# Kernel tuning notes

Hardware: AMD Instinct MI355X
Metric: run time of the kernel (lower is better)

Reference implementation:

```python
import jax, jax.numpy as jnp
import numpy as np

FEAT_STRIDE = 8
IM_DIMS = (4096.0, 4096.0)  # (height, width)
ANCHOR_SCALES = (8.0, 16.0, 32.0)
RATIOS = (0.5, 1.0, 2.0)
PRE_NMS_TOPN = 12000   # TRAIN cfg (eval_mode=False)
POST_NMS_TOPN = 2000
NMS_THRESH = 0.7
MIN_SIZE = 16.0


def _generate_anchors(base_size=16.0, ratios=RATIOS, scales=ANCHOR_SCALES):
    ratios = np.array(ratios, np.float32)
    scales = np.array(scales, np.float32)
    w = h = float(base_size)
    x_ctr = 0.5 * (w - 1.0)
    y_ctr = 0.5 * (h - 1.0)
    size = w * h
    ws = np.round(np.sqrt(size / ratios))
    hs = np.round(ws * ratios)
    out = []
    for wr, hr in zip(ws, hs):
        wss = wr * scales
        hss = hr * scales
        out.append(np.stack([x_ctr - 0.5 * (wss - 1.0), y_ctr - 0.5 * (hss - 1.0),
                             x_ctr + 0.5 * (wss - 1.0), y_ctr + 0.5 * (hss - 1.0)], axis=1))
    return np.concatenate(out, 0).astype(np.float32)  # [A=9, 4]


def _nms(boxes, scores, thresh, max_out):
    # greedy sequential NMS; indices are discrete -> stop gradients here
    boxes = jax.lax.stop_gradient(boxes)
    scores = jax.lax.stop_gradient(scores)
    areas = (boxes[:, 2] - boxes[:, 0] + 1.0) * (boxes[:, 3] - boxes[:, 1] + 1.0)

    def body(i, state):
        supp, keep = state
        idx = jnp.argmax(jnp.where(supp, -jnp.inf, scores))
        b = boxes[idx]
        xx1 = jnp.maximum(b[0], boxes[:, 0])
        yy1 = jnp.maximum(b[1], boxes[:, 1])
        xx2 = jnp.minimum(b[2], boxes[:, 2])
        yy2 = jnp.minimum(b[3], boxes[:, 3])
        inter = jnp.maximum(0.0, xx2 - xx1 + 1.0) * jnp.maximum(0.0, yy2 - yy1 + 1.0)
        iou = inter / (areas[idx] + areas - inter)
        supp = supp | (iou > thresh)  # also suppresses idx itself (iou==1)
        keep = keep.at[i].set(idx.astype(jnp.int32))
        return supp, keep

    supp0 = jnp.zeros(boxes.shape[0], dtype=bool)
    keep0 = jnp.zeros(max_out, dtype=jnp.int32)
    _, keep = jax.lax.fori_loop(0, max_out, body, (supp0, keep0))
    return keep


def reference(rpn_cls_score, rpn_bbox_pred):
    _, H, W, C2 = rpn_cls_score.shape
    A = C2 // 2
    # rpn_softmax: per-anchor 2-way (bg, fg) softmax; channels laid out [2, A]
    prob = jax.nn.softmax(rpn_cls_score.reshape(H, W, 2, A), axis=2)
    scores = prob[:, :, 1, :].reshape(-1)           # fg scores, [H*W*A]
    deltas = rpn_bbox_pred.reshape(-1, 4)           # [H*W*A, 4]

    # anchors shifted over the feature grid
    anchors = jnp.asarray(_generate_anchors())       # [A, 4]
    sx = jnp.arange(W, dtype=jnp.float32) * FEAT_STRIDE
    sy = jnp.arange(H, dtype=jnp.float32) * FEAT_STRIDE
    shift_x, shift_y = jnp.meshgrid(sx, sy)          # [H, W]
    shifts = jnp.stack([shift_x, shift_y, shift_x, shift_y], -1).reshape(-1, 1, 4)
    all_anchors = (anchors[None, :, :] + shifts).reshape(-1, 4)  # [H*W*A, 4]

    # bbox_transform_inv
    ws = all_anchors[:, 2] - all_anchors[:, 0] + 1.0
    hs = all_anchors[:, 3] - all_anchors[:, 1] + 1.0
    cx = all_anchors[:, 0] + 0.5 * ws
    cy = all_anchors[:, 1] + 0.5 * hs
    dx, dy, dw, dh = deltas[:, 0], deltas[:, 1], deltas[:, 2], deltas[:, 3]
    pcx = dx * ws + cx
    pcy = dy * hs + cy
    pw = jnp.exp(dw) * ws
    ph = jnp.exp(dh) * hs
    x1 = pcx - 0.5 * pw
    y1 = pcy - 0.5 * ph
    x2 = pcx + 0.5 * pw
    y2 = pcy + 0.5 * ph

    # clip to image boundaries
    x1 = jnp.clip(x1, 0.0, IM_DIMS[1] - 1.0)
    y1 = jnp.clip(y1, 0.0, IM_DIMS[0] - 1.0)
    x2 = jnp.clip(x2, 0.0, IM_DIMS[1] - 1.0)
    y2 = jnp.clip(y2, 0.0, IM_DIMS[0] - 1.0)
    proposals = jnp.stack([x1, y1, x2, y2], axis=1)

    # drop tiny boxes (jit-friendly: -inf score instead of physical removal)
    keep_min = ((x2 - x1 + 1.0) >= MIN_SIZE) & ((y2 - y1 + 1.0) >= MIN_SIZE)
    scores = jnp.where(keep_min, scores, -jnp.inf)

    top_scores, order = jax.lax.top_k(scores, PRE_NMS_TOPN)
    props = proposals[order]                         # [pre_nms_topN, 4]
    keep = _nms(props, top_scores, NMS_THRESH, POST_NMS_TOPN)
    rois = props[keep]                               # [post_nms_topN, 4]
    # blob: [batch_idx(=0), x1, y1, x2, y2]
    return jnp.concatenate([jnp.zeros((POST_NMS_TOPN, 1), rois.dtype), rois], axis=1)


def setup_inputs() -> dict:
    key = jax.random.key(0)
    k1, k2 = jax.random.split(key)
    rpn_cls_score = jax.random.normal(k1, (1, 512, 512, 18), dtype=jnp.float32)
    rpn_bbox_pred = jax.random.normal(k2, (1, 512, 512, 36), dtype=jnp.float32) * 0.2
    return {"rpn_cls_score": rpn_cls_score, "rpn_bbox_pred": rpn_bbox_pred}
```

## Files before the change

kernel.cpp:

```cpp
#include <hip/hip_runtime.h>
#include <cstdint>
#include <cstddef>

#pragma clang fp contract(off)

#define N_ANCH 2359296
#define K_PRE  12000
#define K_POST 2000
#define NWORD  188
#define TIE_CAP 65536

typedef unsigned int u32;
typedef unsigned long long u64;

__constant__ float c_anch[9][4] = {
  { -84.f,  -40.f,   99.f,   55.f },
  { -176.f, -88.f,  191.f,  103.f },
  { -360.f, -184.f, 375.f,  199.f },
  { -56.f,  -56.f,   71.f,   71.f },
  { -120.f, -120.f, 135.f,  135.f },
  { -248.f, -248.f, 263.f,  263.f },
  { -36.f,  -80.f,   51.f,   95.f },
  { -80.f,  -168.f,  95.f,  183.f },
  { -168.f, -344.f, 183.f,  359.f },
};

__device__ __forceinline__ float pexpf(float xin) {
#pragma clang fp contract(off)
  const float exp_hi = 88.3762626647950f;
  const float exp_lo = -88.3762626647949f;
  const float LOG2EF = 1.44269504088896341f;
  const float C1 = 0.693359375f;
  const float C2 = -2.12194440e-4f;
  const float p0 = 1.9875691500E-4f;
  const float p1 = 1.3981999507E-3f;
  const float p2 = 8.3334519073E-3f;
  const float p3 = 4.1665795894E-2f;
  const float p4 = 1.6666665459E-1f;
  const float p5 = 5.0000001201E-1f;
  float x = fminf(fmaxf(xin, exp_lo), exp_hi);
  float fx = floorf(x * LOG2EF + 0.5f);
  float tmp = C1 * fx;
  float z = C2 * fx;
  x = x - tmp;
  x = x - z;
  z = x * x;
  float y = x * p0 + p1;
  y = y * x + p2;
  y = y * x + p3;
  y = y * x + p4;
  y = y * x + p5;
  y = y * z + x;
  y = 1.0f + y;
  int n = (int)fx;
  u32 e = ((u32)(n + 127)) << 23;
  return y * __uint_as_float(e);
}

__device__ __forceinline__ void decode_box(const float* __restrict__ bbox, int aidx,
                                           float4* ob, float* oarea, bool* okeep) {
#pragma clang fp contract(off)
  int pos = aidx / 9;
  int a = aidx - pos * 9;
  int w = pos & 511;
  int h = pos >> 9;
  float shx = (float)(w * 8);
  float shy = (float)(h * 8);
  float ax1 = c_anch[a][0] + shx;
  float ay1 = c_anch[a][1] + shy;
  float ax2 = c_anch[a][2] + shx;
  float ay2 = c_anch[a][3] + shy;
  float aw = (ax2 - ax1) + 1.0f;
  float ah = (ay2 - ay1) + 1.0f;
  float acx = ax1 + 0.5f * aw;
  float acy = ay1 + 0.5f * ah;
  const float* d = bbox + (size_t)pos * 36 + (size_t)a * 4;
  float dx = d[0], dy = d[1], dw = d[2], dh = d[3];
  float pcx = dx * aw + acx;
  float pcy = dy * ah + acy;
  float pw = pexpf(dw) * aw;
  float ph = pexpf(dh) * ah;
  float x1 = pcx - 0.5f * pw;
  float y1 = pcy - 0.5f * ph;
  float x2 = pcx + 0.5f * pw;
  float y2 = pcy + 0.5f * ph;
  x1 = fminf(fmaxf(x1, 0.0f), 4095.0f);
  y1 = fminf(fmaxf(y1, 0.0f), 4095.0f);
  x2 = fminf(fmaxf(x2, 0.0f), 4095.0f);
  y2 = fminf(fmaxf(y2, 0.0f), 4095.0f);
  *ob = make_float4(x1, y1, x2, y2);
  float ww = (x2 - x1) + 1.0f;
  float hh = (y2 - y1) + 1.0f;
  *oarea = ww * hh;
  *okeep = (ww >= 16.0f) && (hh >= 16.0f);
}

__global__ void k_scores(const float* __restrict__ cls, const float* __restrict__ bbox,
                         u32* __restrict__ keys, u32* __restrict__ ctl,
                         u32* __restrict__ hist) {
#pragma clang fp contract(off)
  int t = blockIdx.x * blockDim.x + threadIdx.x;
  if (blockIdx.x == 0) {
    if (threadIdx.x < 16) ctl[threadIdx.x] = (threadIdx.x == 1) ? (u32)K_PRE : 0u;
    hist[threadIdx.x] = 0u;
  }
  if (t >= N_ANCH) return;
  int pos = t / 9;
  int a = t - pos * 9;
  float s0 = cls[(size_t)pos * 18 + a];
  float s1 = cls[(size_t)pos * 18 + 9 + a];
  float m = fmaxf(s0, s1);
  float e0 = pexpf(s0 - m);
  float e1 = pexpf(s1 - m);
  float p = e1 / (e0 + e1);
  float4 box; float area; bool km;
  decode_box(bbox, t, &box, &area, &km);
  keys[t] = km ? (__float_as_uint(p) | 0x80000000u) : 0u;
}

__global__ void k_histscan(const u32* __restrict__ keys, u32* __restrict__ ctl,
                           u32* __restrict__ hist, int shift, int pass) {
  __shared__ u32 lh[256];
  __shared__ u32 s_last;
  int t = threadIdx.x;
  lh[t] = 0u;
  __syncthreads();
  u32 prefix = ctl[0];
  u32 msk = (shift == 24) ? 0u : (0xFFFFFFFFu << (shift + 8));
  int stride = gridDim.x * blockDim.x;
  for (int i = blockIdx.x * blockDim.x + t; i < N_ANCH; i += stride) {
    u32 k = keys[i];
    if ((k & msk) == prefix) atomicAdd(&lh[(k >> shift) & 0xFFu], 1u);
  }
  __syncthreads();
  if (lh[t]) atomicAdd(&hist[t], lh[t]);
  __syncthreads();
  if (t == 0) {
    __threadfence();
    u32 old = atomicAdd(&ctl[8 + pass], 1u);
    s_last = (old == gridDim.x - 1) ? 1u : 0u;
  }
  __syncthreads();
  if (!s_last) return;
  __threadfence();
  __shared__ u32 sh[256];
  __shared__ u32 horig[256];
  __shared__ int s_d;
  u32 h = atomicAdd(&hist[t], 0u);
  sh[t] = h; horig[t] = h;
  if (t == 0) s_d = 0;
  u32 krem = ctl[1];
  __syncthreads();
  u32 v = h;
  for (int off = 1; off < 256; off <<= 1) {
    u32 add = (t + off < 256) ? sh[t + off] : 0u;
    __syncthreads();
    v += add;
    sh[t] = v;
    __syncthreads();
  }
  if (sh[t] >= krem) atomicMax(&s_d, t);
  __syncthreads();
  if (t == 0) {
    int d = s_d;
    u32 cum = sh[d] - horig[d];
    ctl[0] |= ((u32)d) << shift;
    ctl[1] = krem - cum;
    if (shift == 0) { ctl[2] = ctl[0]; ctl[3] = ctl[1]; }
  }
  hist[t] = 0u;
}

__global__ void k_collect(const u32* __restrict__ keys, u32* __restrict__ ctl,
                          int* __restrict__ sel, int* __restrict__ tie,
                          u64* __restrict__ comps) {
  __shared__ int stI[2048];
  __shared__ u64 stC[2048];
  __shared__ int stT[256];
  __shared__ u32 s_cnt, s_tcnt, s_base, s_tbase;
  int tid = threadIdx.x;
  if (tid == 0) { s_cnt = 0; s_tcnt = 0; }
  __syncthreads();
  u32 kstar = ctl[2];
  int stride = gridDim.x * blockDim.x;
  for (int i = blockIdx.x * blockDim.x + tid; i < N_ANCH; i += stride) {
    u32 k = keys[i];
    if (k > kstar) {
      u32 p = atomicAdd(&s_cnt, 1u);
      u64 cmp = ((u64)k << 32) | (u64)(0xFFFFFFFFu - (u32)i);
      if (p < 2048u) { stI[p] = i; stC[p] = cmp; }
      else { u32 g = atomicAdd(&ctl[4], 1u); sel[g] = i; comps[g] = cmp; }
    } else if (k == kstar) {
      u32 p = atomicAdd(&s_tcnt, 1u);
      if (p < 256u) stT[p] = i;
      else { u32 g = atomicAdd(&ctl[5], 1u); if (g < TIE_CAP) tie[g] = i; }
    }
  }
  __syncthreads();
  if (tid == 0) {
    u32 n = min(s_cnt, 2048u);
    s_base = atomicAdd(&ctl[4], n);
    u32 tn = min(s_tcnt, 256u);
    s_tbase = atomicAdd(&ctl[5], tn);
  }
  __syncthreads();
  u32 n = min(s_cnt, 2048u);
  for (u32 q = tid; q < n; q += blockDim.x) {
    sel[s_base + q] = stI[q];
    comps[s_base + q] = stC[q];
  }
  u32 tn = min(s_tcnt, 256u);
  for (u32 q = tid; q < tn; q += blockDim.x) {
    u32 g = s_tbase + q;
    if (g < TIE_CAP) tie[g] = stT[q];
  }
}

__global__ void k_tiepick(const u32* __restrict__ ctl, const int* __restrict__ tie,
                          int* __restrict__ sel, u64* __restrict__ comps) {
  u32 T = ctl[5]; if (T > TIE_CAP) T = TIE_CAP;
  if (T > 8192u) T = 8192u;
  u32 need = ctl[3];
  u32 base = ctl[4];
  u32 kstar = ctl[2];
  for (u32 t = threadIdx.x; t < T; t += blockDim.x) {
    int v = tie[t];
    u32 r = 0;
    for (u32 u = 0; u < T; ++u) r += (tie[u] < v) ? 1u : 0u;
    if (r < need) {
      sel[base + r] = v;
      comps[base + r] = ((u64)kstar << 32) | (u64)(0xFFFFFFFFu - (u32)v);
    }
  }
}

__global__ void k_rankdec(const u64* __restrict__ comps, const int* __restrict__ sel,
                          const float* __restrict__ bbox,
                          float4* __restrict__ props, float* __restrict__ areas) {
  int lane = threadIdx.x & 63;
  int wave = threadIdx.x >> 6;
  int base = (blockIdx.x * 4 + wave) * 8;
  u64 c0 = comps[base + 0], c1 = comps[base + 1], c2 = comps[base + 2], c3 = comps[base + 3];
  u64 c4 = comps[base + 4], c5 = comps[base + 5], c6 = comps[base + 6], c7 = comps[base + 7];
  int n0 = 0, n1 = 0, n2 = 0, n3 = 0, n4 = 0, n5 = 0, n6 = 0, n7 = 0;
#pragma unroll 4
  for (int j = lane; j < K_PRE; j += 64) {
    u64 v = comps[j];
    n0 += (v > c0); n1 += (v > c1); n2 += (v > c2); n3 += (v > c3);
    n4 += (v > c4); n5 += (v > c5); n6 += (v > c6); n7 += (v > c7);
  }
  for (int off = 32; off; off >>= 1) {
    n0 += __shfl_xor(n0, off); n1 += __shfl_xor(n1, off);
    n2 += __shfl_xor(n2, off); n3 += __shfl_xor(n3, off);
    n4 += __shfl_xor(n4, off); n5 += __shfl_xor(n5, off);
    n6 += __shfl_xor(n6, off); n7 += __shfl_xor(n7, off);
  }
  int rk = n0;
  rk = (lane == 1) ? n1 : rk; rk = (lane == 2) ? n2 : rk;
  rk = (lane == 3) ? n3 : rk; rk = (lane == 4) ? n4 : rk;
  rk = (lane == 5) ? n5 : rk; rk = (lane == 6) ? n6 : rk;
  rk = (lane == 7) ? n7 : rk;
  if (lane < 8) {
    float4 box; float area; bool km;
    decode_box(bbox, sel[base + lane], &box, &area, &km);
    props[rk] = box;
    areas[rk] = area;
  }
}

__global__ void k_mask(const float4* __restrict__ props, const float* __restrict__ areas,
                       u64* __restrict__ mask, u64* __restrict__ diagbuf,
                       u64* __restrict__ subbuf) {
#pragma clang fp contract(off)
  int x = blockIdx.x, y = blockIdx.y;
  if (y + 1 < x || y == x + 1) return;
  __shared__ float4 bj[64];
  __shared__ float aj[64];
  int j0 = y * 64;
  bj[threadIdx.x] = props[j0 + threadIdx.x];
  aj[threadIdx.x] = areas[j0 + threadIdx.x];
  __syncthreads();
  int i = x * 64 + threadIdx.x;
  float4 bi = props[i];
  float ai = areas[i];
  u64 bits = 0;
  for (int jj = 0; jj < 64; ++jj) {
    int j = j0 + jj;
    float4 bb = bj[jj];
    float xx1 = fmaxf(bi.x, bb.x);
    float yy1 = fmaxf(bi.y, bb.y);
    float xx2 = fminf(bi.z, bb.z);
    float yy2 = fminf(bi.w, bb.w);
    float w = fmaxf(0.0f, (xx2 - xx1) + 1.0f);
    float h = fmaxf(0.0f, (yy2 - yy1) + 1.0f);
    float inter = w * h;
    float iou = inter / ((ai + aj[jj]) - inter);
    if ((iou > 0.7f) && (j < K_PRE)) bits |= (1ull << jj);
  }
  if (y == x)          diagbuf[x * 64 + threadIdx.x] = bits;
  else if (y == x - 1) subbuf[x * 64 + threadIdx.x] = bits;
  else                 mask[(size_t)i * NWORD + y] = bits;
}

#define NMS_BAR() asm volatile("s_waitcnt lgkmcnt(0)\n\ts_barrier" ::: "memory")

__global__ void __launch_bounds__(1024) k_nms(const u64* __restrict__ mask,
                                              const u64* __restrict__ diagbuf,
                                              const u64* __restrict__ subbuf,
                                              const float4* __restrict__ props,
                                              float* __restrict__ out) {
  __shared__ u64 rem[NWORD];
  __shared__ int keepb[K_POST];
  __shared__ int kept[2][64];
  __shared__ int s_kk[2];
  __shared__ int s_nk;
  __shared__ int s_brk;
  int tid = threadIdx.x;
  int lane = tid & 63;
  int wave = tid >> 6;
  for (int w = tid; w < NWORD; w += 1024) {
    int base = w * 64;
    u64 v;
    if (base + 64 <= K_PRE) v = 0ull;
    else if (base >= K_PRE) v = ~0ull;
    else v = (~0ull) << (K_PRE - base);
    rem[w] = v;
  }
  if (tid == 0) { s_nk = 0; s_brk = 0; s_kk[0] = 0; s_kk[1] = 0; }
  __syncthreads();

  u64 diagA = 0, diagB = 0, subA = 0, subB = 0;
  if (wave == 0) {
    diagA = diagbuf[lane];
    subA  = subbuf[64 + lane];
  }
  int nk = 0;

  for (int c = 0; c < NWORD; ++c) {
    if (s_brk) break;
    if (wave == 0) {
      if (c + 1 < NWORD) diagB = diagbuf[(c + 1) * 64 + lane];
      subB = (c + 2 < NWORD) ? subbuf[(c + 2) * 64 + lane] : 0ull;
      u64 w = ~rem[c];
      u64 myrow = diagA;
      int kk = 0;
      u64 km = 0;
      while (w != 0ull && nk < K_POST) {
        int j = (int)__builtin_ctzll(w);
        if (lane == 0) { keepb[nk] = (c << 6) | j; kept[c & 1][kk] = (c << 6) | j; }
        km |= (1ull << j);
        nk++; kk++;
        u64 sup = __ballot((int)((myrow >> j) & 1ull));
        w &= ~sup;
        w &= ~(1ull << j);
      }
      if (c + 1 < NWORD) {
        u64 v = __ballot((int)((subA & km) != 0ull));
        if (lane == 0 && v) atomicOr((unsigned long long*)&rem[c + 1], (unsigned long long)v);
      }
      if (lane == 0) {
        s_kk[c & 1] = kk;
        s_nk = nk;
        if (nk >= K_POST) s_brk = 1;
      }
      diagA = diagB; subA = subB;
    } else if (c >= 1) {
      int kkp = s_kk[(c - 1) & 1];
      const int* kb = &kept[(c - 1) & 1][0];
      int wv = wave - 1;
      int nu = kkp * 3;
      for (int b = wv; b < nu; b += 60) {
        int u0 = b, u1 = b + 15, u2 = b + 30, u3 = b + 45;
        u64 p0 = 0, p1 = 0, p2 = 0, p3 = 0;
        int w0 = 0, w1 = 0, w2 = 0, w3 = 0;
        if (u0 < nu) {
          int q = u0 / 3, s = u0 - q * 3;
          int w = c + 1 + s * 64 + lane;
          if (w < NWORD) { w0 = w; p0 = mask[(size_t)kb[q] * NWORD + w]; }
        }
        if (u1 < nu) {
          int q = u1 / 3, s = u1 - q * 3;
          int w = c + 1 + s * 64 + lane;
          if (w < NWORD) { w1 = w; p1 = mask[(size_t)kb[q] * NWORD + w]; }
        }
        if (u2 < nu) {
          int q = u2 / 3, s = u2 - q * 3;
          int w = c + 1 + s * 64 + lane;
          if (w < NWORD) { w2 = w; p2 = mask[(size_t)kb[q] * NWORD + w]; }
        }
        if (u3 < nu) {
          int q = u3 / 3, s = u3 - q * 3;
          int w = c + 1 + s * 64 + lane;
          if (w < NWORD) { w3 = w; p3 = mask[(size_t)kb[q] * NWORD + w]; }
        }
        if (p0) atomicOr((unsigned long long*)&rem[w0], (unsigned long long)p0);
        if (p1) atomicOr((unsigned long long*)&rem[w1], (unsigned long long)p1);
        if (p2) atomicOr((unsigned long long*)&rem[w2], (unsigned long long)p2);
        if (p3) atomicOr((unsigned long long*)&rem[w3], (unsigned long long)p3);
      }
    }
    NMS_BAR();
  }
  __syncthreads();
  int fnk = s_nk;
  for (int t = tid; t < K_POST; t += 1024) {
    int kidx = (t < fnk) ? keepb[t] : 0;
    float4 b = props[kidx];
    out[t * 5 + 0] = 0.0f;
    out[t * 5 + 1] = b.x;
    out[t * 5 + 2] = b.y;
    out[t * 5 + 3] = b.z;
    out[t * 5 + 4] = b.w;
  }
}

extern "C" void kernel_launch(void* const* d_in, const int* in_sizes, int n_in,
                              void* d_out, int out_size, void* d_ws, size_t ws_size,
                              hipStream_t stream) {
  const float* cls  = (const float*)d_in[0];
  const float* bbox = (const float*)d_in[1];
  float* out = (float*)d_out;
  char* ws = (char*)d_ws;

  u64* mask    = (u64*)ws;
  u32* keys    = (u32*)ws;
  u32* ctl     = (u32*)(ws + 9437184);
  u32* hist    = (u32*)(ws + 9437248);
  int* sel     = (int*)(ws + 9438464);
  int* tie     = (int*)(ws + 9486592);
  u64* comps   = (u64*)(ws + 18096128);
  float4* props= (float4*)(ws + 18240512);
  float* areas = (float*)(ws + 18433024);
  u64* diagbuf = (u64*)(ws + 18481152);
  u64* subbuf  = (u64*)(ws + 18577408);

  k_scores<<<dim3((N_ANCH + 255) / 256), dim3(256), 0, stream>>>(cls, bbox, keys, ctl, hist);
  const int shifts[4] = {24, 16, 8, 0};
  for (int s = 0; s < 4; ++s)
    k_histscan<<<dim3(256), dim3(256), 0, stream>>>(keys, ctl, hist, shifts[s], s);
  k_collect<<<dim3(256), dim3(256), 0, stream>>>(keys, ctl, sel, tie, comps);
  k_tiepick<<<dim3(1), dim3(256), 0, stream>>>(ctl, tie, sel, comps);
  k_rankdec<<<dim3(375), dim3(256), 0, stream>>>(comps, sel, bbox, props, areas);
  k_mask<<<dim3(188, 188), dim3(64), 0, stream>>>(props, areas, mask, diagbuf, subbuf);
  k_nms<<<dim3(1), dim3(1024), 0, stream>>>(mask, diagbuf, subbuf, props, out);
}
```

Baseline: 365.3 us.

## Fuse top-byte histogram into scores kernel and process NMS in 128-box chunks

The first radix-select histogram pass (top byte) is folded into k_scores through per-block shared histograms and a last-block scan, which removes one full pass over the keys. Counter initialisation moves to a small k_init kernel. The sequential NMS wave now handles two 64-bit words (128 boxes) per iteration, using 2x2 diagonal and sub-diagonal blocks, which halves the number of barrier-synchronised iterations of the serial loop. In exchange the scores kernel gains atomics and a grid-wide last-block step, and the serial wave does more ballots per iteration.

```diff
diff --git a/kernel.cpp b/kernel.cpp
--- a/kernel.cpp
+++ b/kernel.cpp
@@ -8,6 +8,7 @@
 #define K_PRE  12000
 #define K_POST 2000
 #define NWORD  188
+#define NC     94
 #define TIE_CAP 65536
 
 typedef unsigned int u32;
@@ -95,16 +96,22 @@
   *okeep = (ww >= 16.0f) && (hh >= 16.0f);
 }
 
+__global__ void k_init(u32* __restrict__ ctl, u32* __restrict__ hist) {
+  int t = threadIdx.x;
+  if (t < 16) ctl[t] = (t == 1) ? (u32)K_PRE : 0u;
+  hist[t] = 0u;
+}
+
 __global__ void k_scores(const float* __restrict__ cls, const float* __restrict__ bbox,
                          u32* __restrict__ keys, u32* __restrict__ ctl,
                          u32* __restrict__ hist) {
 #pragma clang fp contract(off)
-  int t = blockIdx.x * blockDim.x + threadIdx.x;
-  if (blockIdx.x == 0) {
-    if (threadIdx.x < 16) ctl[threadIdx.x] = (threadIdx.x == 1) ? (u32)K_PRE : 0u;
-    hist[threadIdx.x] = 0u;
-  }
-  if (t >= N_ANCH) return;
+  __shared__ u32 lh[256];
+  __shared__ u32 s_last;
+  int tid = threadIdx.x;
+  int t = blockIdx.x * blockDim.x + tid;
+  lh[tid] = 0u;
+  __syncthreads();
   int pos = t / 9;
   int a = t - pos * 9;
   float s0 = cls[(size_t)pos * 18 + a];
@@ -115,7 +122,45 @@
   float p = e1 / (e0 + e1);
   float4 box; float area; bool km;
   decode_box(bbox, t, &box, &area, &km);
-  keys[t] = km ? (__float_as_uint(p) | 0x80000000u) : 0u;
+  u32 key = km ? (__float_as_uint(p) | 0x80000000u) : 0u;
+  keys[t] = key;
+  atomicAdd(&lh[key >> 24], 1u);
+  __syncthreads();
+  if (lh[tid]) atomicAdd(&hist[tid], lh[tid]);
+  __syncthreads();
+  if (tid == 0) {
+    __threadfence();
+    u32 old = atomicAdd(&ctl[15], 1u);
+    s_last = (old == gridDim.x - 1) ? 1u : 0u;
+  }
+  __syncthreads();
+  if (!s_last) return;
+  __threadfence();
+  __shared__ u32 sh[256];
+  __shared__ u32 horig[256];
+  __shared__ int s_d;
+  u32 h = atomicAdd(&hist[tid], 0u);
+  sh[tid] = h; horig[tid] = h;
+  if (tid == 0) s_d = 0;
+  u32 krem = ctl[1];
+  __syncthreads();
+  u32 v = h;
+  for (int off = 1; off < 256; off <<= 1) {
+    u32 add = (tid + off < 256) ? sh[tid + off] : 0u;
+    __syncthreads();
+    v += add;
+    sh[tid] = v;
+    __syncthreads();
+  }
+  if (sh[tid] >= krem) atomicMax(&s_d, tid);
+  __syncthreads();
+  if (tid == 0) {
+    int d = s_d;
+    u32 cum = sh[d] - horig[d];
+    ctl[0] |= ((u32)d) << 24;
+    ctl[1] = krem - cum;
+  }
+  hist[tid] = 0u;
 }
 
 __global__ void k_histscan(const u32* __restrict__ keys, u32* __restrict__ ctl,
@@ -126,7 +171,7 @@
   lh[t] = 0u;
   __syncthreads();
   u32 prefix = ctl[0];
-  u32 msk = (shift == 24) ? 0u : (0xFFFFFFFFu << (shift + 8));
+  u32 msk = 0xFFFFFFFFu << (shift + 8);
   int stride = gridDim.x * blockDim.x;
   for (int i = blockIdx.x * blockDim.x + t; i < N_ANCH; i += stride) {
     u32 k = keys[i];
@@ -268,12 +313,17 @@
   }
 }
 
+__device__ __forceinline__ int d2idx(int c, int h, int lane) {
+  return ((c * 2 + h) * 64 + lane) * 2;
+}
+
 __global__ void k_mask(const float4* __restrict__ props, const float* __restrict__ areas,
-                       u64* __restrict__ mask, u64* __restrict__ diagbuf,
-                       u64* __restrict__ subbuf) {
+                       u64* __restrict__ mask, u64* __restrict__ diag2,
+                       u64* __restrict__ sub2) {
 #pragma clang fp contract(off)
   int x = blockIdx.x, y = blockIdx.y;
-  if (y + 1 < x || y == x + 1) return;
+  int cx = x >> 1, cy = y >> 1;
+  if (cy + 1 < cx || cy == cx + 1) return;
   __shared__ float4 bj[64];
   __shared__ float aj[64];
   int j0 = y * 64;
@@ -297,21 +347,21 @@
     float iou = inter / ((ai + aj[jj]) - inter);
     if ((iou > 0.7f) && (j < K_PRE)) bits |= (1ull << jj);
   }
-  if (y == x)          diagbuf[x * 64 + threadIdx.x] = bits;
-  else if (y == x - 1) subbuf[x * 64 + threadIdx.x] = bits;
-  else                 mask[(size_t)i * NWORD + y] = bits;
+  if (cy == cx)          diag2[d2idx(cx, x & 1, threadIdx.x) + (y & 1)] = bits;
+  else if (cy == cx - 1) sub2[d2idx(cx, x & 1, threadIdx.x) + (y & 1)] = bits;
+  else                   mask[(size_t)i * NWORD + y] = bits;
 }
 
 #define NMS_BAR() asm volatile("s_waitcnt lgkmcnt(0)\n\ts_barrier" ::: "memory")
 
 __global__ void __launch_bounds__(1024) k_nms(const u64* __restrict__ mask,
-                                              const u64* __restrict__ diagbuf,
-                                              const u64* __restrict__ subbuf,
+                                              const u64* __restrict__ diag2,
+                                              const u64* __restrict__ sub2,
                                               const float4* __restrict__ props,
                                               float* __restrict__ out) {
   __shared__ u64 rem[NWORD];
   __shared__ int keepb[K_POST];
-  __shared__ int kept[2][64];
+  __shared__ int kept[2][128];
   __shared__ int s_kk[2];
   __shared__ int s_nk;
   __shared__ int s_brk;
@@ -329,45 +379,76 @@
   if (tid == 0) { s_nk = 0; s_brk = 0; s_kk[0] = 0; s_kk[1] = 0; }
   __syncthreads();
 
-  u64 diagA = 0, diagB = 0, subA = 0, subB = 0;
+  u64 dl0A = 0, dl1A = 0, dh0A = 0, dh1A = 0;
+  u64 sl0A = 0, sl1A = 0, sh0A = 0, sh1A = 0;
+  u64 dl0B = 0, dl1B = 0, dh0B = 0, dh1B = 0;
+  u64 sl0B = 0, sl1B = 0, sh0B = 0, sh1B = 0;
   if (wave == 0) {
-    diagA = diagbuf[lane];
-    subA  = subbuf[64 + lane];
+    const u64* p;
+    p = diag2 + d2idx(0, 0, lane); dl0A = p[0]; dl1A = p[1];
+    p = diag2 + d2idx(0, 1, lane); dh0A = p[0]; dh1A = p[1];
+    p = sub2 + d2idx(1, 0, lane);  sl0A = p[0]; sl1A = p[1];
+    p = sub2 + d2idx(1, 1, lane);  sh0A = p[0]; sh1A = p[1];
   }
   int nk = 0;
 
-  for (int c = 0; c < NWORD; ++c) {
+  for (int c = 0; c < NC; ++c) {
     if (s_brk) break;
+    int par = c & 1;
     if (wave == 0) {
-      if (c + 1 < NWORD) diagB = diagbuf[(c + 1) * 64 + lane];
-      subB = (c + 2 < NWORD) ? subbuf[(c + 2) * 64 + lane] : 0ull;
-      u64 w = ~rem[c];
-      u64 myrow = diagA;
+      if (c + 1 < NC) {
+        const u64* p = diag2 + d2idx(c + 1, 0, lane); dl0B = p[0]; dl1B = p[1];
+        p = diag2 + d2idx(c + 1, 1, lane); dh0B = p[0]; dh1B = p[1];
+      }
+      if (c + 2 < NC) {
+        const u64* p = sub2 + d2idx(c + 2, 0, lane); sl0B = p[0]; sl1B = p[1];
+        p = sub2 + d2idx(c + 2, 1, lane); sh0B = p[0]; sh1B = p[1];
+      } else { sl0B = sl1B = sh0B = sh1B = 0ull; }
+      u64 w0 = ~rem[2 * c];
+      u64 w1 = ~rem[2 * c + 1];
+      u64 km0 = 0, km1 = 0;
       int kk = 0;
-      u64 km = 0;
-      while (w != 0ull && nk < K_POST) {
-        int j = (int)__builtin_ctzll(w);
-        if (lane == 0) { keepb[nk] = (c << 6) | j; kept[c & 1][kk] = (c << 6) | j; }
-        km |= (1ull << j);
+      while (w0 != 0ull && nk < K_POST) {
+        int j = (int)__builtin_ctzll(w0);
+        int blo = (int)((dl0A >> j) & 1ull);
+        int bhi = (int)((dh0A >> j) & 1ull);
+        u64 suplo = __ballot(blo);
+        u64 suphi = __ballot(bhi);
+        if (lane == 0) { keepb[nk] = (c << 7) | j; kept[par][kk] = (c << 7) | j; }
         nk++; kk++;
-        u64 sup = __ballot((int)((myrow >> j) & 1ull));
-        w &= ~sup;
-        w &= ~(1ull << j);
+        km0 |= (1ull << j);
+        w0 &= ~suplo;
+        w1 &= ~suphi;
+        w0 &= ~(1ull << j);
       }
-      if (c + 1 < NWORD) {
-        u64 v = __ballot((int)((subA & km) != 0ull));
-        if (lane == 0 && v) atomicOr((unsigned long long*)&rem[c + 1], (unsigned long long)v);
+      while (w1 != 0ull && nk < K_POST) {
+        int j = (int)__builtin_ctzll(w1);
+        int bhi = (int)((dh1A >> j) & 1ull);
+        u64 suphi = __ballot(bhi);
+        if (lane == 0) { keepb[nk] = (c << 7) | 64 | j; kept[par][kk] = (c << 7) | 64 | j; }
+        nk++; kk++;
+        km1 |= (1ull << j);
+        w1 &= ~suphi;
+        w1 &= ~(1ull << j);
       }
-      if (lane == 0) {
-        s_kk[c & 1] = kk;
-        s_nk = nk;
-        if (nk >= K_POST) s_brk = 1;
+      if (c + 1 < NC) {
+        int plo = (int)((((sl0A & km0) | (sl1A & km1)) != 0ull) ? 1 : 0);
+        int phi = (int)((((sh0A & km0) | (sh1A & km1)) != 0ull) ? 1 : 0);
+        u64 vlo = __ballot(plo);
+        u64 vhi = __ballot(phi);
+        if (lane == 0) {
+          if (vlo) atomicOr((unsigned long long*)&rem[2 * c + 2], (unsigned long long)vlo);
+          if (vhi) atomicOr((unsigned long long*)&rem[2 * c + 3], (unsigned long long)vhi);
+        }
       }
-      diagA = diagB; subA = subB;
+      if (lane == 0) { s_kk[par] = kk; s_nk = nk; s_brk = (nk >= K_POST) ? 1 : 0; }
+      dl0A = dl0B; dl1A = dl1B; dh0A = dh0B; dh1A = dh1B;
+      sl0A = sl0B; sl1A = sl1B; sh0A = sh0B; sh1A = sh1B;
     } else if (c >= 1) {
-      int kkp = s_kk[(c - 1) & 1];
-      const int* kb = &kept[(c - 1) & 1][0];
+      int kkp = s_kk[par ^ 1];
+      const int* kb = &kept[par ^ 1][0];
       int wv = wave - 1;
+      int B = 2 * c + 2;
       int nu = kkp * 3;
       for (int b = wv; b < nu; b += 60) {
         int u0 = b, u1 = b + 15, u2 = b + 30, u3 = b + 45;
@@ -375,22 +456,22 @@
         int w0 = 0, w1 = 0, w2 = 0, w3 = 0;
         if (u0 < nu) {
           int q = u0 / 3, s = u0 - q * 3;
-          int w = c + 1 + s * 64 + lane;
+          int w = B + s * 64 + lane;
           if (w < NWORD) { w0 = w; p0 = mask[(size_t)kb[q] * NWORD + w]; }
         }
         if (u1 < nu) {
           int q = u1 / 3, s = u1 - q * 3;
-          int w = c + 1 + s * 64 + lane;
+          int w = B + s * 64 + lane;
           if (w < NWORD) { w1 = w; p1 = mask[(size_t)kb[q] * NWORD + w]; }
         }
         if (u2 < nu) {
           int q = u2 / 3, s = u2 - q * 3;
-          int w = c + 1 + s * 64 + lane;
+          int w = B + s * 64 + lane;
           if (w < NWORD) { w2 = w; p2 = mask[(size_t)kb[q] * NWORD + w]; }
         }
         if (u3 < nu) {
           int q = u3 / 3, s = u3 - q * 3;
-          int w = c + 1 + s * 64 + lane;
+          int w = B + s * 64 + lane;
           if (w < NWORD) { w3 = w; p3 = mask[(size_t)kb[q] * NWORD + w]; }
         }
         if (p0) atomicOr((unsigned long long*)&rem[w0], (unsigned long long)p0);
@@ -431,16 +512,17 @@
   u64* comps   = (u64*)(ws + 18096128);
   float4* props= (float4*)(ws + 18240512);
   float* areas = (float*)(ws + 18433024);
-  u64* diagbuf = (u64*)(ws + 18481152);
-  u64* subbuf  = (u64*)(ws + 18577408);
-
-  k_scores<<<dim3((N_ANCH + 255) / 256), dim3(256), 0, stream>>>(cls, bbox, keys, ctl, hist);
-  const int shifts[4] = {24, 16, 8, 0};
-  for (int s = 0; s < 4; ++s)
+  u64* diag2   = (u64*)(ws + 18481152);
+  u64* sub2    = (u64*)(ws + 18673664);
+
+  k_init<<<dim3(1), dim3(256), 0, stream>>>(ctl, hist);
+  k_scores<<<dim3(N_ANCH / 256), dim3(256), 0, stream>>>(cls, bbox, keys, ctl, hist);
+  const int shifts[3] = {16, 8, 0};
+  for (int s = 0; s < 3; ++s)
     k_histscan<<<dim3(256), dim3(256), 0, stream>>>(keys, ctl, hist, shifts[s], s);
   k_collect<<<dim3(256), dim3(256), 0, stream>>>(keys, ctl, sel, tie, comps);
   k_tiepick<<<dim3(1), dim3(256), 0, stream>>>(ctl, tie, sel, comps);
   k_rankdec<<<dim3(375), dim3(256), 0, stream>>>(comps, sel, bbox, props, areas);
-  k_mask<<<dim3(188, 188), dim3(64), 0, stream>>>(props, areas, mask, diagbuf, subbuf);
-  k_nms<<<dim3(1), dim3(1024), 0, stream>>>(mask, diagbuf, subbuf, props, out);
-}
+  k_mask<<<dim3(188, 188), dim3(64), 0, stream>>>(props, areas, mask, diag2, sub2);
+  k_nms<<<dim3(1), dim3(1024), 0, stream>>>(mask, diag2, sub2, props, out);
+}
```

Result: slower. 608.7 us (+66.6%).
